# Optimization experiments

Hardware: AMD Instinct MI355X
Metric: run time of the kernel (lower is better)

## Reference

```python
import jax, jax.numpy as jnp
import numpy as np

INPUT_SIZE = 64
HIDDEN = 128
NUM_CLASSES = 4
BATCH = 512
SEQ = 1024


def setup_inputs() -> dict:
    key = jax.random.key(0)
    ks = jax.random.split(key, 11)
    s_in = 1.0 / np.sqrt(INPUT_SIZE)
    s_h = 1.0 / np.sqrt(HIDDEN)
    inp = {
        "x": jax.random.normal(ks[0], (BATCH, SEQ, INPUT_SIZE), dtype=jnp.float32),
        # layer1: x_proj (4H, in), h_proj (4H, H), each with bias
        "Wx1": jax.random.uniform(ks[1], (4 * HIDDEN, INPUT_SIZE), minval=-s_in, maxval=s_in),
        "bx1": jax.random.uniform(ks[2], (4 * HIDDEN,), minval=-s_in, maxval=s_in),
        "Wh1": jax.random.uniform(ks[3], (4 * HIDDEN, HIDDEN), minval=-s_h, maxval=s_h),
        "bh1": jax.random.uniform(ks[4], (4 * HIDDEN,), minval=-s_h, maxval=s_h),
        # layer2: x_proj (4H, H), h_proj (4H, H)
        "Wx2": jax.random.uniform(ks[5], (4 * HIDDEN, HIDDEN), minval=-s_h, maxval=s_h),
        "bx2": jax.random.uniform(ks[6], (4 * HIDDEN,), minval=-s_h, maxval=s_h),
        "Wh2": jax.random.uniform(ks[7], (4 * HIDDEN, HIDDEN), minval=-s_h, maxval=s_h),
        "bh2": jax.random.uniform(ks[8], (4 * HIDDEN,), minval=-s_h, maxval=s_h),
        # classifier head (num_classes, H)
        "Wc": jax.random.uniform(ks[9], (NUM_CLASSES, HIDDEN), minval=-s_h, maxval=s_h),
        "bc": jax.random.uniform(ks[10], (NUM_CLASSES,), minval=-s_h, maxval=s_h),
    }
    return inp


def _cell(gates, c_prev):
    # torch Linear gate order after chunk(4): i, f, g, o
    i, f, g, o = jnp.split(gates, 4, axis=-1)
    c = jax.nn.sigmoid(f) * c_prev + jax.nn.sigmoid(i) * jnp.tanh(g)
    h = jax.nn.sigmoid(o) * jnp.tanh(c)
    return h, c


def reference(x, Wx1, bx1, Wh1, bh1, Wx2, bx2, Wh2, bh2, Wc, bc):
    B = x.shape[0]
    H = Wh1.shape[1]
    # Precompute input projections for all timesteps in one big GEMM: (B,S,4H)
    xg1 = jnp.einsum("bsi,gi->bsg", x, Wx1) + bx1 + bh1  # fold both biases
    xg1_t = jnp.swapaxes(xg1, 0, 1)  # (S, B, 4H) for scan

    def step(carry, xg_t):
        h1, c1, h2, c2 = carry
        gates1 = xg_t + h1 @ Wh1.T
        h1, c1 = _cell(gates1, c1)
        gates2 = h1 @ Wx2.T + bx2 + h2 @ Wh2.T + bh2
        h2, c2 = _cell(gates2, c2)
        return (h1, c1, h2, c2), None

    z = jnp.zeros((B, H), dtype=x.dtype)
    (h1, c1, h2, c2), _ = jax.lax.scan(step, (z, z, z, z), xg1_t)
    logits = h2 @ Wc.T + bc  # (B, num_classes)
    return logits
```

## Files before the change

### kernel.cpp

```cpp
#include <hip/hip_runtime.h>
#include <hip/hip_fp16.h>

namespace {

constexpr int kS = 1024;
constexpr int kI = 64;
constexpr int kH = 128;

typedef _Float16 f16x8 __attribute__((ext_vector_type(8)));
typedef float    f32x4 __attribute__((ext_vector_type(4)));

#define MFMA16(a, b, c) __builtin_amdgcn_mfma_f32_16x16x32_f16((a), (b), (c), 0, 0, 0)

__device__ __forceinline__ float rcpf(float x) {
#if __has_builtin(__builtin_amdgcn_rcpf)
  return __builtin_amdgcn_rcpf(x);
#else
  return 1.0f / x;
#endif
}
__device__ __forceinline__ float sigf(float x)  { return rcpf(1.0f + __expf(-x)); }
__device__ __forceinline__ float tanhff(float x){ return 1.0f - 2.0f * rcpf(1.0f + __expf(2.0f * x)); }

template <int P>
__device__ __forceinline__ void prio() {
#if __has_builtin(__builtin_amdgcn_s_setprio)
  __builtin_amdgcn_s_setprio(P);
#endif
}

__device__ __forceinline__ unsigned packf2(float lo, float hi) {
  _Float16 a = (_Float16)lo, b = (_Float16)hi;
  unsigned short ua = __builtin_bit_cast(unsigned short, a);
  unsigned short ub = __builtin_bit_cast(unsigned short, b);
  return (unsigned)ua | ((unsigned)ub << 16);
}

__device__ __forceinline__ f16x8 afrag(const float* __restrict__ W, int row,
                                       int k0, int ld) {
  const float4* p = reinterpret_cast<const float4*>(W + (size_t)row * ld + k0);
  const float4 u = p[0], v = p[1];
  f16x8 a;
  a[0] = (_Float16)u.x; a[1] = (_Float16)u.y; a[2] = (_Float16)u.z; a[3] = (_Float16)u.w;
  a[4] = (_Float16)v.x; a[5] = (_Float16)v.y; a[6] = (_Float16)v.z; a[7] = (_Float16)v.w;
  return a;
}

__global__ __launch_bounds__(1024) void lstm_l1(
    const float* __restrict__ x, const float* __restrict__ Wx1,
    const float* __restrict__ bx1, const float* __restrict__ Wh1,
    const float* __restrict__ bh1, _Float16* __restrict__ h1out)
{
  const int tid  = threadIdx.x;
  const int b0   = blockIdx.x * 2;
  const int w    = tid >> 6;
  const int lane = tid & 63;
  const int q    = lane >> 4;
  const int n    = lane & 15;

  __shared__ __align__(16) _Float16 xF[8][16][8];
  __shared__ __align__(16) _Float16 h1B[2][2][16][8];
  __shared__ float xg[512][17];
  __shared__ float gbuf[2][512];

  f16x8 Ax[2][2], Ah[2][4];
  {
    const int rb = w * 32 + n;
#pragma unroll
    for (int s = 0; s < 2; ++s) {
      const int row = rb + s * 16;
#pragma unroll
      for (int kt = 0; kt < 2; ++kt) Ax[s][kt] = afrag(Wx1, row, kt * 32 + q * 8, kI);
#pragma unroll
      for (int kt = 0; kt < 4; ++kt) Ah[s][kt] = afrag(Wh1, row, kt * 32 + q * 8, kH);
    }
  }

  float bI = 0.f, bF = 0.f, bG = 0.f, bO = 0.f, cst = 0.f;
  if (tid < 256) {
    const int j = tid & 127;
    bI = bx1[j]       + bh1[j];
    bF = bx1[j + 128] + bh1[j + 128];
    bG = bx1[j + 256] + bh1[j + 256];
    bO = bx1[j + 384] + bh1[j + 384];
    reinterpret_cast<_Float16*>(&h1B[1][0][0][0])[tid] = (_Float16)0.f;
  }

  const int csel  = (n < 2) ? n : 0;
  const char* h1base = reinterpret_cast<const char*>(&h1B[0][0][0][0]);

  for (int t0 = 0; t0 < kS; t0 += 8) {
    if (tid < 512) {
      const int col = tid >> 5, sk2 = tid & 31;
      const int c = col & 1, dt = col >> 1;
      const float2 v = *reinterpret_cast<const float2*>(
          x + ((size_t)(b0 + c) * kS + (size_t)(t0 + dt)) * kI + sk2 * 2);
      const int k = sk2 * 2;
      *reinterpret_cast<unsigned*>(&xF[k >> 3][col][k & 7]) = packf2(v.x, v.y);
    }
    __syncthreads();

    {
      const char* xb = reinterpret_cast<const char*>(&xF[0][0][0]);
      f32x4 e0 = {0.f, 0.f, 0.f, 0.f}, e1 = {0.f, 0.f, 0.f, 0.f};
#pragma unroll
      for (int kt = 0; kt < 2; ++kt) {
        const f16x8 bf = *reinterpret_cast<const f16x8*>(
            xb + (((kt * 4 + q) * 16 + n) << 4));
        e0 = MFMA16(Ax[0][kt], bf, e0);
        e1 = MFMA16(Ax[1][kt], bf, e1);
      }
#pragma unroll
      for (int r = 0; r < 4; ++r) {
        xg[w * 32 + q * 4 + r][n]      = e0[r];
        xg[w * 32 + 16 + q * 4 + r][n] = e1[r];
      }
    }
    __syncthreads();

    for (int dt = 0; dt < 8; ++dt) {
      const int t = t0 + dt;
      const int rp = (t + 1) & 1;
      const char* hb = h1base + ((rp * 2 + csel) << 8);

      f32x4 d0 = {0.f, 0.f, 0.f, 0.f}, d1 = {0.f, 0.f, 0.f, 0.f};
      prio<1>();
#pragma unroll
      for (int kt = 0; kt < 4; ++kt) {
        const f16x8 bf = *reinterpret_cast<const f16x8*>(hb + ((kt * 4 + q) << 4));
        d0 = MFMA16(Ah[0][kt], bf, d0);
        d1 = MFMA16(Ah[1][kt], bf, d1);
      }
      prio<0>();

      if (n < 2) {
        *reinterpret_cast<f32x4*>(&gbuf[n][w * 32 + q * 4])      = d0;
        *reinterpret_cast<f32x4*>(&gbuf[n][w * 32 + 16 + q * 4]) = d1;
      }
      __syncthreads();

      if (tid < 256) {
        const int c = tid >> 7, j = tid & 127, col = dt * 2 + c;
        const float gi = xg[j][col]       + gbuf[c][j]       + bI;
        const float gf = xg[j + 128][col] + gbuf[c][j + 128] + bF;
        const float gg = xg[j + 256][col] + gbuf[c][j + 256] + bG;
        const float go = xg[j + 384][col] + gbuf[c][j + 384] + bO;
        cst = sigf(gf) * cst + sigf(gi) * tanhff(gg);
        const float h = sigf(go) * tanhff(cst);
        h1B[t & 1][c][j >> 3][j & 7] = (_Float16)h;
        h1out[((size_t)(b0 + c) * kS + (size_t)t) * kH + j] = (_Float16)h;
      }
      __syncthreads();
    }
  }
}

__global__ __launch_bounds__(1024) void lstm_l2(
    const _Float16* __restrict__ h1in,
    const float* __restrict__ Wx2, const float* __restrict__ bx2,
    const float* __restrict__ Wh2, const float* __restrict__ bh2,
    const float* __restrict__ Wc,  const float* __restrict__ bc,
    float* __restrict__ out)
{
  const int tid  = threadIdx.x;
  const int b0   = blockIdx.x * 2;
  const int w    = tid >> 6;
  const int lane = tid & 63;
  const int q    = lane >> 4;
  const int n    = lane & 15;

  __shared__ __align__(16) _Float16 h1F[16][16][8];
  __shared__ __align__(16) _Float16 h2B[2][2][16][8];
  __shared__ float xg[512][17];
  __shared__ float gbuf[2][512];
  __shared__ float hfin[2][128];

  f16x8 Ax[2][4], Ah[2][4];
  {
    const int rb = w * 32 + n;
#pragma unroll
    for (int s = 0; s < 2; ++s) {
      const int row = rb + s * 16;
#pragma unroll
      for (int kt = 0; kt < 4; ++kt) {
        Ax[s][kt] = afrag(Wx2, row, kt * 32 + q * 8, kH);
        Ah[s][kt] = afrag(Wh2, row, kt * 32 + q * 8, kH);
      }
    }
  }

  float bI = 0.f, bF = 0.f, bG = 0.f, bO = 0.f, cst = 0.f;
  if (tid < 256) {
    const int j = tid & 127;
    bI = bx2[j]       + bh2[j];
    bF = bx2[j + 128] + bh2[j + 128];
    bG = bx2[j + 256] + bh2[j + 256];
    bO = bx2[j + 384] + bh2[j + 384];
    reinterpret_cast<_Float16*>(&h2B[1][0][0][0])[tid] = (_Float16)0.f;
  }

  const int csel = (n < 2) ? n : 0;
  const char* h2base = reinterpret_cast<const char*>(&h2B[0][0][0][0]);

  for (int t0 = 0; t0 < kS; t0 += 8) {
    {
      const int col = tid >> 6, sk2 = tid & 63;
      const int c = col & 1, dt = col >> 1;
      const unsigned v = *reinterpret_cast<const unsigned*>(
          h1in + ((size_t)(b0 + c) * kS + (size_t)(t0 + dt)) * kH + sk2 * 2);
      const int k = sk2 * 2;
      *reinterpret_cast<unsigned*>(&h1F[k >> 3][col][k & 7]) = v;
    }
    __syncthreads();

    {
      const char* xb = reinterpret_cast<const char*>(&h1F[0][0][0]);
      f32x4 e0 = {0.f, 0.f, 0.f, 0.f}, e1 = {0.f, 0.f, 0.f, 0.f};
#pragma unroll
      for (int kt = 0; kt < 4; ++kt) {
        const f16x8 bf = *reinterpret_cast<const f16x8*>(
            xb + (((kt * 4 + q) * 16 + n) << 4));
        e0 = MFMA16(Ax[0][kt], bf, e0);
        e1 = MFMA16(Ax[1][kt], bf, e1);
      }
#pragma unroll
      for (int r = 0; r < 4; ++r) {
        xg[w * 32 + q * 4 + r][n]      = e0[r];
        xg[w * 32 + 16 + q * 4 + r][n] = e1[r];
      }
    }
    __syncthreads();

    for (int dt = 0; dt < 8; ++dt) {
      const int t = t0 + dt;
      const int rp = (t + 1) & 1;
      const char* hb = h2base + ((rp * 2 + csel) << 8);

      f32x4 d0 = {0.f, 0.f, 0.f, 0.f}, d1 = {0.f, 0.f, 0.f, 0.f};
      prio<1>();
#pragma unroll
      for (int kt = 0; kt < 4; ++kt) {
        const f16x8 bf = *reinterpret_cast<const f16x8*>(hb + ((kt * 4 + q) << 4));
        d0 = MFMA16(Ah[0][kt], bf, d0);
        d1 = MFMA16(Ah[1][kt], bf, d1);
      }
      prio<0>();

      if (n < 2) {
        *reinterpret_cast<f32x4*>(&gbuf[n][w * 32 + q * 4])      = d0;
        *reinterpret_cast<f32x4*>(&gbuf[n][w * 32 + 16 + q * 4]) = d1;
      }
      __syncthreads();

      if (tid < 256) {
        const int c = tid >> 7, j = tid & 127, col = dt * 2 + c;
        const float gi = xg[j][col]       + gbuf[c][j]       + bI;
        const float gf = xg[j + 128][col] + gbuf[c][j + 128] + bF;
        const float gg = xg[j + 256][col] + gbuf[c][j + 256] + bG;
        const float go = xg[j + 384][col] + gbuf[c][j + 384] + bO;
        cst = sigf(gf) * cst + sigf(gi) * tanhff(gg);
        const float h = sigf(go) * tanhff(cst);
        h2B[t & 1][c][j >> 3][j & 7] = (_Float16)h;
        if (t == kS - 1) hfin[c][j] = h;
      }
      __syncthreads();
    }
  }

  if (tid < 8) {
    const int m = tid & 3, c = tid >> 2;
    const float* wr = Wc + (size_t)m * kH;
    float s0 = 0.f, s1 = 0.f, s2 = 0.f, s3 = 0.f;
#pragma unroll
    for (int j = 0; j < kH; j += 4) {
      s0 = fmaf(wr[j],     hfin[c][j],     s0);
      s1 = fmaf(wr[j + 1], hfin[c][j + 1], s1);
      s2 = fmaf(wr[j + 2], hfin[c][j + 2], s2);
      s3 = fmaf(wr[j + 3], hfin[c][j + 3], s3);
    }
    out[(size_t)(b0 + c) * 4 + m] = bc[m] + ((s0 + s1) + (s2 + s3));
  }
}

}

extern "C" void kernel_launch(void* const* d_in, const int* in_sizes, int n_in,
                              void* d_out, int out_size, void* d_ws, size_t ws_size,
                              hipStream_t stream) {
  const float* x   = (const float*)d_in[0];
  const float* Wx1 = (const float*)d_in[1];
  const float* bx1 = (const float*)d_in[2];
  const float* Wh1 = (const float*)d_in[3];
  const float* bh1 = (const float*)d_in[4];
  const float* Wx2 = (const float*)d_in[5];
  const float* bx2 = (const float*)d_in[6];
  const float* Wh2 = (const float*)d_in[7];
  const float* bh2 = (const float*)d_in[8];
  const float* Wc  = (const float*)d_in[9];
  const float* bc  = (const float*)d_in[10];

  _Float16* h1 = (_Float16*)d_ws;

  hipLaunchKernelGGL(lstm_l1, dim3(256), dim3(1024), 0, stream,
                     x, Wx1, bx1, Wh1, bh1, h1);
  hipLaunchKernelGGL(lstm_l2, dim3(256), dim3(1024), 0, stream,
                     h1, Wx2, bx2, Wh2, bh2, Wc, bc, (float*)d_out);
}
```

Measured before the change: 1.537 ms.

## Remap gate rows per wave so each lane owns i,f,g,o and drop a barrier

Each block drops from 16 to 8 waves, and each wave now computes all four gates for the same 16 hidden units. The lanes holding the MFMA output can then apply the LSTM cell directly in registers, without staging gate sums through shared memory and a second barrier per timestep. The precomputed input projection is stored transposed so each lane reads its four values as one vector, and the s_setprio hints are removed. In exchange, each wave holds twice as many weight fragments in registers, and only the lanes with n<2 run the elementwise math, so each of them does four hidden units serially.

```diff
diff --git a/kernel.cpp b/kernel.cpp
--- a/kernel.cpp
+++ b/kernel.cpp
@@ -21,13 +21,6 @@
 }
 __device__ __forceinline__ float sigf(float x)  { return rcpf(1.0f + __expf(-x)); }
 __device__ __forceinline__ float tanhff(float x){ return 1.0f - 2.0f * rcpf(1.0f + __expf(2.0f * x)); }
-
-template <int P>
-__device__ __forceinline__ void prio() {
-#if __has_builtin(__builtin_amdgcn_s_setprio)
-  __builtin_amdgcn_s_setprio(P);
-#endif
-}
 
 __device__ __forceinline__ unsigned packf2(float lo, float hi) {
   _Float16 a = (_Float16)lo, b = (_Float16)hi;
@@ -46,7 +39,8 @@
   return a;
 }
 
-__global__ __launch_bounds__(1024) void lstm_l1(
+
+__global__ __launch_bounds__(512) void lstm_l1(
     const float* __restrict__ x, const float* __restrict__ Wx1,
     const float* __restrict__ bx1, const float* __restrict__ Wh1,
     const float* __restrict__ bh1, _Float16* __restrict__ h1out)
@@ -57,105 +51,104 @@
   const int lane = tid & 63;
   const int q    = lane >> 4;
   const int n    = lane & 15;
+  const int j0   = 16 * w + 4 * q;
 
   __shared__ __align__(16) _Float16 xF[8][16][8];
   __shared__ __align__(16) _Float16 h1B[2][2][16][8];
-  __shared__ float xg[512][17];
-  __shared__ float gbuf[2][512];
-
-  f16x8 Ax[2][2], Ah[2][4];
-  {
-    const int rb = w * 32 + n;
-#pragma unroll
-    for (int s = 0; s < 2; ++s) {
-      const int row = rb + s * 16;
-#pragma unroll
-      for (int kt = 0; kt < 2; ++kt) Ax[s][kt] = afrag(Wx1, row, kt * 32 + q * 8, kI);
-#pragma unroll
-      for (int kt = 0; kt < 4; ++kt) Ah[s][kt] = afrag(Wh1, row, kt * 32 + q * 8, kH);
-    }
-  }
-
-  float bI = 0.f, bF = 0.f, bG = 0.f, bO = 0.f, cst = 0.f;
-  if (tid < 256) {
-    const int j = tid & 127;
-    bI = bx1[j]       + bh1[j];
-    bF = bx1[j + 128] + bh1[j + 128];
-    bG = bx1[j + 256] + bh1[j + 256];
-    bO = bx1[j + 384] + bh1[j + 384];
-    reinterpret_cast<_Float16*>(&h1B[1][0][0][0])[tid] = (_Float16)0.f;
-  }
-
-  const int csel  = (n < 2) ? n : 0;
+  __shared__ float xg2[16][516];
+
+  f16x8 Ax[4][2], Ah[4][4];
+#pragma unroll
+  for (int g = 0; g < 4; ++g) {
+    const int row = g * 128 + 16 * w + n;
+#pragma unroll
+    for (int kt = 0; kt < 2; ++kt) Ax[g][kt] = afrag(Wx1, row, kt * 32 + q * 8, kI);
+#pragma unroll
+    for (int kt = 0; kt < 4; ++kt) Ah[g][kt] = afrag(Wh1, row, kt * 32 + q * 8, kH);
+  }
+
+  f32x4 bI4, bF4, bG4, bO4;
+#pragma unroll
+  for (int r = 0; r < 4; ++r) {
+    bI4[r] = bx1[j0 + r]       + bh1[j0 + r];
+    bF4[r] = bx1[j0 + 128 + r] + bh1[j0 + 128 + r];
+    bG4[r] = bx1[j0 + 256 + r] + bh1[j0 + 256 + r];
+    bO4[r] = bx1[j0 + 384 + r] + bh1[j0 + 384 + r];
+  }
+  if (tid < 256) reinterpret_cast<_Float16*>(&h1B[1][0][0][0])[tid] = (_Float16)0.f;
+
+  f32x4 cst = {0.f, 0.f, 0.f, 0.f};
+  const int csel = (n < 2) ? n : 0;
   const char* h1base = reinterpret_cast<const char*>(&h1B[0][0][0][0]);
 
   for (int t0 = 0; t0 < kS; t0 += 8) {
-    if (tid < 512) {
-      const int col = tid >> 5, sk2 = tid & 31;
-      const int c = col & 1, dt = col >> 1;
+    {
+      const int col = tid >> 5, k2 = tid & 31;
+      const int c = col & 1, dt = col >> 1, k = k2 * 2;
       const float2 v = *reinterpret_cast<const float2*>(
-          x + ((size_t)(b0 + c) * kS + (size_t)(t0 + dt)) * kI + sk2 * 2);
-      const int k = sk2 * 2;
+          x + ((size_t)(b0 + c) * kS + (size_t)(t0 + dt)) * kI + k);
       *reinterpret_cast<unsigned*>(&xF[k >> 3][col][k & 7]) = packf2(v.x, v.y);
     }
     __syncthreads();
 
     {
       const char* xb = reinterpret_cast<const char*>(&xF[0][0][0]);
-      f32x4 e0 = {0.f, 0.f, 0.f, 0.f}, e1 = {0.f, 0.f, 0.f, 0.f};
+      f32x4 e0 = {0,0,0,0}, e1 = {0,0,0,0}, e2 = {0,0,0,0}, e3 = {0,0,0,0};
 #pragma unroll
       for (int kt = 0; kt < 2; ++kt) {
         const f16x8 bf = *reinterpret_cast<const f16x8*>(
             xb + (((kt * 4 + q) * 16 + n) << 4));
-        e0 = MFMA16(Ax[0][kt], bf, e0);
-        e1 = MFMA16(Ax[1][kt], bf, e1);
-      }
-#pragma unroll
-      for (int r = 0; r < 4; ++r) {
-        xg[w * 32 + q * 4 + r][n]      = e0[r];
-        xg[w * 32 + 16 + q * 4 + r][n] = e1[r];
-      }
+        e0 = MFMA16(Ax[0][kt], bf, e0);  e1 = MFMA16(Ax[1][kt], bf, e1);
+        e2 = MFMA16(Ax[2][kt], bf, e2);  e3 = MFMA16(Ax[3][kt], bf, e3);
+      }
+      *reinterpret_cast<f32x4*>(&xg2[n][j0])       = e0;
+      *reinterpret_cast<f32x4*>(&xg2[n][j0 + 128]) = e1;
+      *reinterpret_cast<f32x4*>(&xg2[n][j0 + 256]) = e2;
+      *reinterpret_cast<f32x4*>(&xg2[n][j0 + 384]) = e3;
     }
     __syncthreads();
 
     for (int dt = 0; dt < 8; ++dt) {
       const int t = t0 + dt;
-      const int rp = (t + 1) & 1;
-      const char* hb = h1base + ((rp * 2 + csel) << 8);
-
-      f32x4 d0 = {0.f, 0.f, 0.f, 0.f}, d1 = {0.f, 0.f, 0.f, 0.f};
-      prio<1>();
+      const char* hb = h1base + ((((t + 1) & 1) * 2 + csel) << 8);
+
+      f32x4 d0 = {0,0,0,0}, d1 = {0,0,0,0}, d2 = {0,0,0,0}, d3 = {0,0,0,0};
 #pragma unroll
       for (int kt = 0; kt < 4; ++kt) {
         const f16x8 bf = *reinterpret_cast<const f16x8*>(hb + ((kt * 4 + q) << 4));
-        d0 = MFMA16(Ah[0][kt], bf, d0);
-        d1 = MFMA16(Ah[1][kt], bf, d1);
-      }
-      prio<0>();
+        d0 = MFMA16(Ah[0][kt], bf, d0);  d1 = MFMA16(Ah[1][kt], bf, d1);
+        d2 = MFMA16(Ah[2][kt], bf, d2);  d3 = MFMA16(Ah[3][kt], bf, d3);
+      }
 
       if (n < 2) {
-        *reinterpret_cast<f32x4*>(&gbuf[n][w * 32 + q * 4])      = d0;
-        *reinterpret_cast<f32x4*>(&gbuf[n][w * 32 + 16 + q * 4]) = d1;
+        const int col = dt * 2 + n;
+        const f32x4 xa  = *reinterpret_cast<const f32x4*>(&xg2[col][j0]);
+        const f32x4 xf  = *reinterpret_cast<const f32x4*>(&xg2[col][j0 + 128]);
+        const f32x4 xgg = *reinterpret_cast<const f32x4*>(&xg2[col][j0 + 256]);
+        const f32x4 xo  = *reinterpret_cast<const f32x4*>(&xg2[col][j0 + 384]);
+        float h[4];
+#pragma unroll
+        for (int r = 0; r < 4; ++r) {
+          const float gi = d0[r] + xa[r]  + bI4[r];
+          const float gf = d1[r] + xf[r]  + bF4[r];
+          const float gg = d2[r] + xgg[r] + bG4[r];
+          const float go = d3[r] + xo[r]  + bO4[r];
+          cst[r] = sigf(gf) * cst[r] + sigf(gi) * tanhff(gg);
+          h[r] = sigf(go) * tanhff(cst[r]);
+        }
+        uint2 hp;
+        hp.x = packf2(h[0], h[1]);
+        hp.y = packf2(h[2], h[3]);
+        *reinterpret_cast<uint2*>(&h1B[t & 1][n][j0 >> 3][j0 & 7]) = hp;
+        *reinterpret_cast<uint2*>(
+            h1out + ((size_t)(b0 + n) * kS + (size_t)t) * kH + j0) = hp;
       }
       __syncthreads();
-
-      if (tid < 256) {
-        const int c = tid >> 7, j = tid & 127, col = dt * 2 + c;
-        const float gi = xg[j][col]       + gbuf[c][j]       + bI;
-        const float gf = xg[j + 128][col] + gbuf[c][j + 128] + bF;
-        const float gg = xg[j + 256][col] + gbuf[c][j + 256] + bG;
-        const float go = xg[j + 384][col] + gbuf[c][j + 384] + bO;
-        cst = sigf(gf) * cst + sigf(gi) * tanhff(gg);
-        const float h = sigf(go) * tanhff(cst);
-        h1B[t & 1][c][j >> 3][j & 7] = (_Float16)h;
-        h1out[((size_t)(b0 + c) * kS + (size_t)t) * kH + j] = (_Float16)h;
-      }
-      __syncthreads();
-    }
-  }
-}
-
-__global__ __launch_bounds__(1024) void lstm_l2(
+    }
+  }
+}
+
+__global__ __launch_bounds__(512) void lstm_l2(
     const _Float16* __restrict__ h1in,
     const float* __restrict__ Wx2, const float* __restrict__ bx2,
     const float* __restrict__ Wh2, const float* __restrict__ bh2,
@@ -168,100 +161,101 @@
   const int lane = tid & 63;
   const int q    = lane >> 4;
   const int n    = lane & 15;
+  const int j0   = 16 * w + 4 * q;
 
   __shared__ __align__(16) _Float16 h1F[16][16][8];
   __shared__ __align__(16) _Float16 h2B[2][2][16][8];
-  __shared__ float xg[512][17];
-  __shared__ float gbuf[2][512];
+  __shared__ float xg2[16][516];
   __shared__ float hfin[2][128];
 
-  f16x8 Ax[2][4], Ah[2][4];
-  {
-    const int rb = w * 32 + n;
-#pragma unroll
-    for (int s = 0; s < 2; ++s) {
-      const int row = rb + s * 16;
-#pragma unroll
-      for (int kt = 0; kt < 4; ++kt) {
-        Ax[s][kt] = afrag(Wx2, row, kt * 32 + q * 8, kH);
-        Ah[s][kt] = afrag(Wh2, row, kt * 32 + q * 8, kH);
-      }
-    }
-  }
-
-  float bI = 0.f, bF = 0.f, bG = 0.f, bO = 0.f, cst = 0.f;
-  if (tid < 256) {
-    const int j = tid & 127;
-    bI = bx2[j]       + bh2[j];
-    bF = bx2[j + 128] + bh2[j + 128];
-    bG = bx2[j + 256] + bh2[j + 256];
-    bO = bx2[j + 384] + bh2[j + 384];
-    reinterpret_cast<_Float16*>(&h2B[1][0][0][0])[tid] = (_Float16)0.f;
-  }
-
+  f16x8 Ax[4][4], Ah[4][4];
+#pragma unroll
+  for (int g = 0; g < 4; ++g) {
+    const int row = g * 128 + 16 * w + n;
+#pragma unroll
+    for (int kt = 0; kt < 4; ++kt) {
+      Ax[g][kt] = afrag(Wx2, row, kt * 32 + q * 8, kH);
+      Ah[g][kt] = afrag(Wh2, row, kt * 32 + q * 8, kH);
+    }
+  }
+
+  f32x4 bI4, bF4, bG4, bO4;
+#pragma unroll
+  for (int r = 0; r < 4; ++r) {
+    bI4[r] = bx2[j0 + r]       + bh2[j0 + r];
+    bF4[r] = bx2[j0 + 128 + r] + bh2[j0 + 128 + r];
+    bG4[r] = bx2[j0 + 256 + r] + bh2[j0 + 256 + r];
+    bO4[r] = bx2[j0 + 384 + r] + bh2[j0 + 384 + r];
+  }
+  if (tid < 256) reinterpret_cast<_Float16*>(&h2B[1][0][0][0])[tid] = (_Float16)0.f;
+
+  f32x4 cst = {0.f, 0.f, 0.f, 0.f};
   const int csel = (n < 2) ? n : 0;
   const char* h2base = reinterpret_cast<const char*>(&h2B[0][0][0][0]);
 
   for (int t0 = 0; t0 < kS; t0 += 8) {
     {
-      const int col = tid >> 6, sk2 = tid & 63;
-      const int c = col & 1, dt = col >> 1;
-      const unsigned v = *reinterpret_cast<const unsigned*>(
-          h1in + ((size_t)(b0 + c) * kS + (size_t)(t0 + dt)) * kH + sk2 * 2);
-      const int k = sk2 * 2;
-      *reinterpret_cast<unsigned*>(&h1F[k >> 3][col][k & 7]) = v;
+      const int col = tid >> 5, quad = tid & 31;
+      const int c = col & 1, dt = col >> 1, k = quad * 4;
+      const uint2 v = *reinterpret_cast<const uint2*>(
+          h1in + ((size_t)(b0 + c) * kS + (size_t)(t0 + dt)) * kH + k);
+      *reinterpret_cast<uint2*>(&h1F[k >> 3][col][k & 7]) = v;
     }
     __syncthreads();
 
     {
       const char* xb = reinterpret_cast<const char*>(&h1F[0][0][0]);
-      f32x4 e0 = {0.f, 0.f, 0.f, 0.f}, e1 = {0.f, 0.f, 0.f, 0.f};
+      f32x4 e0 = {0,0,0,0}, e1 = {0,0,0,0}, e2 = {0,0,0,0}, e3 = {0,0,0,0};
 #pragma unroll
       for (int kt = 0; kt < 4; ++kt) {
         const f16x8 bf = *reinterpret_cast<const f16x8*>(
             xb + (((kt * 4 + q) * 16 + n) << 4));
-        e0 = MFMA16(Ax[0][kt], bf, e0);
-        e1 = MFMA16(Ax[1][kt], bf, e1);
-      }
-#pragma unroll
-      for (int r = 0; r < 4; ++r) {
-        xg[w * 32 + q * 4 + r][n]      = e0[r];
-        xg[w * 32 + 16 + q * 4 + r][n] = e1[r];
-      }
+        e0 = MFMA16(Ax[0][kt], bf, e0);  e1 = MFMA16(Ax[1][kt], bf, e1);
+        e2 = MFMA16(Ax[2][kt], bf, e2);  e3 = MFMA16(Ax[3][kt], bf, e3);
+      }
+      *reinterpret_cast<f32x4*>(&xg2[n][j0])       = e0;
+      *reinterpret_cast<f32x4*>(&xg2[n][j0 + 128]) = e1;
+      *reinterpret_cast<f32x4*>(&xg2[n][j0 + 256]) = e2;
+      *reinterpret_cast<f32x4*>(&xg2[n][j0 + 384]) = e3;
     }
     __syncthreads();
 
     for (int dt = 0; dt < 8; ++dt) {
       const int t = t0 + dt;
-      const int rp = (t + 1) & 1;
-      const char* hb = h2base + ((rp * 2 + csel) << 8);
-
-      f32x4 d0 = {0.f, 0.f, 0.f, 0.f}, d1 = {0.f, 0.f, 0.f, 0.f};
-      prio<1>();
+      const char* hb = h2base + ((((t + 1) & 1) * 2 + csel) << 8);
+
+      f32x4 d0 = {0,0,0,0}, d1 = {0,0,0,0}, d2 = {0,0,0,0}, d3 = {0,0,0,0};
 #pragma unroll
       for (int kt = 0; kt < 4; ++kt) {
         const f16x8 bf = *reinterpret_cast<const f16x8*>(hb + ((kt * 4 + q) << 4));
-        d0 = MFMA16(Ah[0][kt], bf, d0);
-        d1 = MFMA16(Ah[1][kt], bf, d1);
-      }
-      prio<0>();
+        d0 = MFMA16(Ah[0][kt], bf, d0);  d1 = MFMA16(Ah[1][kt], bf, d1);
+        d2 = MFMA16(Ah[2][kt], bf, d2);  d3 = MFMA16(Ah[3][kt], bf, d3);
+      }
 
       if (n < 2) {
-        *reinterpret_cast<f32x4*>(&gbuf[n][w * 32 + q * 4])      = d0;
-        *reinterpret_cast<f32x4*>(&gbuf[n][w * 32 + 16 + q * 4]) = d1;
-      }
-      __syncthreads();
-
-      if (tid < 256) {
-        const int c = tid >> 7, j = tid & 127, col = dt * 2 + c;
-        const float gi = xg[j][col]       + gbuf[c][j]       + bI;
-        const float gf = xg[j + 128][col] + gbuf[c][j + 128] + bF;
-        const float gg = xg[j + 256][col] + gbuf[c][j + 256] + bG;
-        const float go = xg[j + 384][col] + gbuf[c][j + 384] + bO;
-        cst = sigf(gf) * cst + sigf(gi) * tanhff(gg);
-        const float h = sigf(go) * tanhff(cst);
-        h2B[t & 1][c][j >> 3][j & 7] = (_Float16)h;
-        if (t == kS - 1) hfin[c][j] = h;
+        const int col = dt * 2 + n;
+        const f32x4 xa  = *reinterpret_cast<const f32x4*>(&xg2[col][j0]);
+        const f32x4 xf  = *reinterpret_cast<const f32x4*>(&xg2[col][j0 + 128]);
+        const f32x4 xgg = *reinterpret_cast<const f32x4*>(&xg2[col][j0 + 256]);
+        const f32x4 xo  = *reinterpret_cast<const f32x4*>(&xg2[col][j0 + 384]);
+        float h[4];
+#pragma unroll
+        for (int r = 0; r < 4; ++r) {
+          const float gi = d0[r] + xa[r]  + bI4[r];
+          const float gf = d1[r] + xf[r]  + bF4[r];
+          const float gg = d2[r] + xgg[r] + bG4[r];
+          const float go = d3[r] + xo[r]  + bO4[r];
+          cst[r] = sigf(gf) * cst[r] + sigf(gi) * tanhff(gg);
+          h[r] = sigf(go) * tanhff(cst[r]);
+        }
+        uint2 hp;
+        hp.x = packf2(h[0], h[1]);
+        hp.y = packf2(h[2], h[3]);
+        *reinterpret_cast<uint2*>(&h2B[t & 1][n][j0 >> 3][j0 & 7]) = hp;
+        if (t == kS - 1) {
+          f32x4 hv = {h[0], h[1], h[2], h[3]};
+          *reinterpret_cast<f32x4*>(&hfin[n][j0]) = hv;
+        }
       }
       __syncthreads();
     }
@@ -301,8 +295,8 @@
 
   _Float16* h1 = (_Float16*)d_ws;
 
-  hipLaunchKernelGGL(lstm_l1, dim3(256), dim3(1024), 0, stream,
+  hipLaunchKernelGGL(lstm_l1, dim3(256), dim3(512), 0, stream,
                      x, Wx1, bx1, Wh1, bh1, h1);
-  hipLaunchKernelGGL(lstm_l2, dim3(256), dim3(1024), 0, stream,
+  hipLaunchKernelGGL(lstm_l2, dim3(256), dim3(512), 0, stream,
                      h1, Wx2, bx2, Wh2, bh2, Wc, bc, (float*)d_out);
 }
```

Result: slower. 2.151 ms (+40.0%).

## Fuse both LSTM layers into one wavefront-specialized kernel with layer-2 lagging one chunk

Applied to the files above, without the earlier changes.

Merges the two per-layer kernels into a single kernel. Waves 0-7 run layer 1 and waves 8-15 run layer 2, with layer 2 one 8-step chunk behind. Layer-1 hidden states pass through shared memory instead of a global fp16 buffer, and each step's two recurrences share the same barriers. This removes the global round-trip of h1 and roughly halves the number of serial barrier-bound steps. In exchange, each wave now holds more recurrent weight fragments in registers, the input-projection weights are reloaded from global memory every chunk, and the setprio hints are dropped.

```diff
diff --git a/kernel.cpp b/kernel.cpp
--- a/kernel.cpp
+++ b/kernel.cpp
@@ -21,20 +21,6 @@
 }
 __device__ __forceinline__ float sigf(float x)  { return rcpf(1.0f + __expf(-x)); }
 __device__ __forceinline__ float tanhff(float x){ return 1.0f - 2.0f * rcpf(1.0f + __expf(2.0f * x)); }
-
-template <int P>
-__device__ __forceinline__ void prio() {
-#if __has_builtin(__builtin_amdgcn_s_setprio)
-  __builtin_amdgcn_s_setprio(P);
-#endif
-}
-
-__device__ __forceinline__ unsigned packf2(float lo, float hi) {
-  _Float16 a = (_Float16)lo, b = (_Float16)hi;
-  unsigned short ua = __builtin_bit_cast(unsigned short, a);
-  unsigned short ub = __builtin_bit_cast(unsigned short, b);
-  return (unsigned)ua | ((unsigned)ub << 16);
-}
 
 __device__ __forceinline__ f16x8 afrag(const float* __restrict__ W, int row,
                                        int k0, int ld) {
@@ -46,117 +32,11 @@
   return a;
 }
 
-__global__ __launch_bounds__(1024) void lstm_l1(
-    const float* __restrict__ x, const float* __restrict__ Wx1,
-    const float* __restrict__ bx1, const float* __restrict__ Wh1,
-    const float* __restrict__ bh1, _Float16* __restrict__ h1out)
-{
-  const int tid  = threadIdx.x;
-  const int b0   = blockIdx.x * 2;
-  const int w    = tid >> 6;
-  const int lane = tid & 63;
-  const int q    = lane >> 4;
-  const int n    = lane & 15;
-
-  __shared__ __align__(16) _Float16 xF[8][16][8];
-  __shared__ __align__(16) _Float16 h1B[2][2][16][8];
-  __shared__ float xg[512][17];
-  __shared__ float gbuf[2][512];
-
-  f16x8 Ax[2][2], Ah[2][4];
-  {
-    const int rb = w * 32 + n;
-#pragma unroll
-    for (int s = 0; s < 2; ++s) {
-      const int row = rb + s * 16;
-#pragma unroll
-      for (int kt = 0; kt < 2; ++kt) Ax[s][kt] = afrag(Wx1, row, kt * 32 + q * 8, kI);
-#pragma unroll
-      for (int kt = 0; kt < 4; ++kt) Ah[s][kt] = afrag(Wh1, row, kt * 32 + q * 8, kH);
-    }
-  }
-
-  float bI = 0.f, bF = 0.f, bG = 0.f, bO = 0.f, cst = 0.f;
-  if (tid < 256) {
-    const int j = tid & 127;
-    bI = bx1[j]       + bh1[j];
-    bF = bx1[j + 128] + bh1[j + 128];
-    bG = bx1[j + 256] + bh1[j + 256];
-    bO = bx1[j + 384] + bh1[j + 384];
-    reinterpret_cast<_Float16*>(&h1B[1][0][0][0])[tid] = (_Float16)0.f;
-  }
-
-  const int csel  = (n < 2) ? n : 0;
-  const char* h1base = reinterpret_cast<const char*>(&h1B[0][0][0][0]);
-
-  for (int t0 = 0; t0 < kS; t0 += 8) {
-    if (tid < 512) {
-      const int col = tid >> 5, sk2 = tid & 31;
-      const int c = col & 1, dt = col >> 1;
-      const float2 v = *reinterpret_cast<const float2*>(
-          x + ((size_t)(b0 + c) * kS + (size_t)(t0 + dt)) * kI + sk2 * 2);
-      const int k = sk2 * 2;
-      *reinterpret_cast<unsigned*>(&xF[k >> 3][col][k & 7]) = packf2(v.x, v.y);
-    }
-    __syncthreads();
-
-    {
-      const char* xb = reinterpret_cast<const char*>(&xF[0][0][0]);
-      f32x4 e0 = {0.f, 0.f, 0.f, 0.f}, e1 = {0.f, 0.f, 0.f, 0.f};
-#pragma unroll
-      for (int kt = 0; kt < 2; ++kt) {
-        const f16x8 bf = *reinterpret_cast<const f16x8*>(
-            xb + (((kt * 4 + q) * 16 + n) << 4));
-        e0 = MFMA16(Ax[0][kt], bf, e0);
-        e1 = MFMA16(Ax[1][kt], bf, e1);
-      }
-#pragma unroll
-      for (int r = 0; r < 4; ++r) {
-        xg[w * 32 + q * 4 + r][n]      = e0[r];
-        xg[w * 32 + 16 + q * 4 + r][n] = e1[r];
-      }
-    }
-    __syncthreads();
-
-    for (int dt = 0; dt < 8; ++dt) {
-      const int t = t0 + dt;
-      const int rp = (t + 1) & 1;
-      const char* hb = h1base + ((rp * 2 + csel) << 8);
-
-      f32x4 d0 = {0.f, 0.f, 0.f, 0.f}, d1 = {0.f, 0.f, 0.f, 0.f};
-      prio<1>();
-#pragma unroll
-      for (int kt = 0; kt < 4; ++kt) {
-        const f16x8 bf = *reinterpret_cast<const f16x8*>(hb + ((kt * 4 + q) << 4));
-        d0 = MFMA16(Ah[0][kt], bf, d0);
-        d1 = MFMA16(Ah[1][kt], bf, d1);
-      }
-      prio<0>();
-
-      if (n < 2) {
-        *reinterpret_cast<f32x4*>(&gbuf[n][w * 32 + q * 4])      = d0;
-        *reinterpret_cast<f32x4*>(&gbuf[n][w * 32 + 16 + q * 4]) = d1;
-      }
-      __syncthreads();
-
-      if (tid < 256) {
-        const int c = tid >> 7, j = tid & 127, col = dt * 2 + c;
-        const float gi = xg[j][col]       + gbuf[c][j]       + bI;
-        const float gf = xg[j + 128][col] + gbuf[c][j + 128] + bF;
-        const float gg = xg[j + 256][col] + gbuf[c][j + 256] + bG;
-        const float go = xg[j + 384][col] + gbuf[c][j + 384] + bO;
-        cst = sigf(gf) * cst + sigf(gi) * tanhff(gg);
-        const float h = sigf(go) * tanhff(cst);
-        h1B[t & 1][c][j >> 3][j & 7] = (_Float16)h;
-        h1out[((size_t)(b0 + c) * kS + (size_t)t) * kH + j] = (_Float16)h;
-      }
-      __syncthreads();
-    }
-  }
-}
-
-__global__ __launch_bounds__(1024) void lstm_l2(
-    const _Float16* __restrict__ h1in,
+__global__ __launch_bounds__(1024, 1) __attribute__((amdgpu_waves_per_eu(4, 4)))
+void lstm_fused(
+    const float* __restrict__ x,
+    const float* __restrict__ Wx1, const float* __restrict__ bx1,
+    const float* __restrict__ Wh1, const float* __restrict__ bh1,
     const float* __restrict__ Wx2, const float* __restrict__ bx2,
     const float* __restrict__ Wh2, const float* __restrict__ bh2,
     const float* __restrict__ Wc,  const float* __restrict__ bc,
@@ -168,100 +48,154 @@
   const int lane = tid & 63;
   const int q    = lane >> 4;
   const int n    = lane & 15;
-
-  __shared__ __align__(16) _Float16 h1F[16][16][8];
+  const int lw   = w & 7;
+  const bool isL2w = (w >= 8);
+  const int csel = (n < 2) ? n : 0;
+
+  __shared__ __align__(16) _Float16 xF[8][17][8];
+  __shared__ __align__(16) _Float16 h1R[2][16][17][8];
   __shared__ __align__(16) _Float16 h2B[2][2][16][8];
-  __shared__ float xg[512][17];
-  __shared__ float gbuf[2][512];
+  __shared__ float xg1[16][516];
+  __shared__ float xg2[16][516];
+  __shared__ float g1[2][512];
+  __shared__ float g2[2][512];
   __shared__ float hfin[2][128];
 
-  f16x8 Ax[2][4], Ah[2][4];
+  f16x8 Ah[4][4];
   {
-    const int rb = w * 32 + n;
-#pragma unroll
-    for (int s = 0; s < 2; ++s) {
-      const int row = rb + s * 16;
-#pragma unroll
-      for (int kt = 0; kt < 4; ++kt) {
-        Ax[s][kt] = afrag(Wx2, row, kt * 32 + q * 8, kH);
-        Ah[s][kt] = afrag(Wh2, row, kt * 32 + q * 8, kH);
-      }
-    }
+    const float* Wr = isL2w ? Wh2 : Wh1;
+#pragma unroll
+    for (int i = 0; i < 4; ++i)
+#pragma unroll
+      for (int kt = 0; kt < 4; ++kt)
+        Ah[i][kt] = afrag(Wr, (lw * 4 + i) * 16 + n, kt * 32 + q * 8, kH);
   }
 
   float bI = 0.f, bF = 0.f, bG = 0.f, bO = 0.f, cst = 0.f;
   if (tid < 256) {
+    const int j = tid & 127;
+    bI = bx1[j]       + bh1[j];
+    bF = bx1[j + 128] + bh1[j + 128];
+    bG = bx1[j + 256] + bh1[j + 256];
+    bO = bx1[j + 384] + bh1[j + 384];
+  } else if (tid >= 512 && tid < 768) {
     const int j = tid & 127;
     bI = bx2[j]       + bh2[j];
     bF = bx2[j + 128] + bh2[j + 128];
     bG = bx2[j + 256] + bh2[j + 256];
     bO = bx2[j + 384] + bh2[j + 384];
-    reinterpret_cast<_Float16*>(&h2B[1][0][0][0])[tid] = (_Float16)0.f;
-  }
-
-  const int csel = (n < 2) ? n : 0;
-  const char* h2base = reinterpret_cast<const char*>(&h2B[0][0][0][0]);
-
-  for (int t0 = 0; t0 < kS; t0 += 8) {
-    {
-      const int col = tid >> 6, sk2 = tid & 63;
+  }
+
+  for (int i = tid; i < 16 * 17 * 8; i += 1024)
+    (&h1R[1][0][0][0])[i] = (_Float16)0.f;
+  if (tid < 512) (&h2B[0][0][0][0])[tid] = (_Float16)0.f;
+
+  for (int T = 0; T < 129; ++T) {
+    const bool hasL1 = (T < 128);
+    const bool hasL2 = (T > 0);
+
+    if (hasL1) {
+      const int col = tid >> 6, k = tid & 63;
       const int c = col & 1, dt = col >> 1;
-      const unsigned v = *reinterpret_cast<const unsigned*>(
-          h1in + ((size_t)(b0 + c) * kS + (size_t)(t0 + dt)) * kH + sk2 * 2);
-      const int k = sk2 * 2;
-      *reinterpret_cast<unsigned*>(&h1F[k >> 3][col][k & 7]) = v;
+      xF[k >> 3][col][k & 7] =
+          (_Float16)x[((size_t)(b0 + c) * kS + (size_t)(T * 8 + dt)) * kI + k];
     }
     __syncthreads();
 
-    {
-      const char* xb = reinterpret_cast<const char*>(&h1F[0][0][0]);
-      f32x4 e0 = {0.f, 0.f, 0.f, 0.f}, e1 = {0.f, 0.f, 0.f, 0.f};
+    if (!isL2w && hasL1) {
+      f32x4 e0 = {0,0,0,0}, e1 = {0,0,0,0}, e2 = {0,0,0,0}, e3 = {0,0,0,0};
+      const char* xb = reinterpret_cast<const char*>(&xF[0][0][0]);
+#pragma unroll
+      for (int kt = 0; kt < 2; ++kt) {
+        const f16x8 bf = *reinterpret_cast<const f16x8*>(
+            xb + (((kt * 4 + q) * 17 + n) << 4));
+        e0 = MFMA16(afrag(Wx1, (lw*4+0)*16 + n, kt*32 + q*8, kI), bf, e0);
+        e1 = MFMA16(afrag(Wx1, (lw*4+1)*16 + n, kt*32 + q*8, kI), bf, e1);
+        e2 = MFMA16(afrag(Wx1, (lw*4+2)*16 + n, kt*32 + q*8, kI), bf, e2);
+        e3 = MFMA16(afrag(Wx1, (lw*4+3)*16 + n, kt*32 + q*8, kI), bf, e3);
+      }
+      *reinterpret_cast<f32x4*>(&xg1[n][(lw*4+0)*16 + q*4]) = e0;
+      *reinterpret_cast<f32x4*>(&xg1[n][(lw*4+1)*16 + q*4]) = e1;
+      *reinterpret_cast<f32x4*>(&xg1[n][(lw*4+2)*16 + q*4]) = e2;
+      *reinterpret_cast<f32x4*>(&xg1[n][(lw*4+3)*16 + q*4]) = e3;
+    }
+    if (isL2w && hasL2) {
+      f32x4 e0 = {0,0,0,0}, e1 = {0,0,0,0}, e2 = {0,0,0,0}, e3 = {0,0,0,0};
+      const char* hb = reinterpret_cast<const char*>(&h1R[(T + 1) & 1][0][0][0]);
 #pragma unroll
       for (int kt = 0; kt < 4; ++kt) {
         const f16x8 bf = *reinterpret_cast<const f16x8*>(
-            xb + (((kt * 4 + q) * 16 + n) << 4));
-        e0 = MFMA16(Ax[0][kt], bf, e0);
-        e1 = MFMA16(Ax[1][kt], bf, e1);
-      }
-#pragma unroll
-      for (int r = 0; r < 4; ++r) {
-        xg[w * 32 + q * 4 + r][n]      = e0[r];
-        xg[w * 32 + 16 + q * 4 + r][n] = e1[r];
-      }
+            hb + (((kt * 4 + q) * 17 + n) << 4));
+        e0 = MFMA16(afrag(Wx2, (lw*4+0)*16 + n, kt*32 + q*8, kH), bf, e0);
+        e1 = MFMA16(afrag(Wx2, (lw*4+1)*16 + n, kt*32 + q*8, kH), bf, e1);
+        e2 = MFMA16(afrag(Wx2, (lw*4+2)*16 + n, kt*32 + q*8, kH), bf, e2);
+        e3 = MFMA16(afrag(Wx2, (lw*4+3)*16 + n, kt*32 + q*8, kH), bf, e3);
+      }
+      *reinterpret_cast<f32x4*>(&xg2[n][(lw*4+0)*16 + q*4]) = e0;
+      *reinterpret_cast<f32x4*>(&xg2[n][(lw*4+1)*16 + q*4]) = e1;
+      *reinterpret_cast<f32x4*>(&xg2[n][(lw*4+2)*16 + q*4]) = e2;
+      *reinterpret_cast<f32x4*>(&xg2[n][(lw*4+3)*16 + q*4]) = e3;
     }
     __syncthreads();
 
     for (int dt = 0; dt < 8; ++dt) {
-      const int t = t0 + dt;
-      const int rp = (t + 1) & 1;
-      const char* hb = h2base + ((rp * 2 + csel) << 8);
-
-      f32x4 d0 = {0.f, 0.f, 0.f, 0.f}, d1 = {0.f, 0.f, 0.f, 0.f};
-      prio<1>();
-#pragma unroll
-      for (int kt = 0; kt < 4; ++kt) {
-        const f16x8 bf = *reinterpret_cast<const f16x8*>(hb + ((kt * 4 + q) << 4));
-        d0 = MFMA16(Ah[0][kt], bf, d0);
-        d1 = MFMA16(Ah[1][kt], bf, d1);
-      }
-      prio<0>();
-
-      if (n < 2) {
-        *reinterpret_cast<f32x4*>(&gbuf[n][w * 32 + q * 4])      = d0;
-        *reinterpret_cast<f32x4*>(&gbuf[n][w * 32 + 16 + q * 4]) = d1;
+      const int t  = T * 8 + dt;
+      const int t2 = t - 8;
+
+      if (!isL2w && hasL1) {
+        const int rb  = (dt == 0) ? ((T + 1) & 1) : (T & 1);
+        const int col = (dt == 0) ? (14 + csel) : ((dt - 1) * 2 + csel);
+        const char* hb = reinterpret_cast<const char*>(&h1R[rb][0][0][0]) + col * 16;
+        f32x4 d0 = {0,0,0,0}, d1 = {0,0,0,0}, d2 = {0,0,0,0}, d3 = {0,0,0,0};
+#pragma unroll
+        for (int kt = 0; kt < 4; ++kt) {
+          const f16x8 bf = *reinterpret_cast<const f16x8*>(hb + (kt * 4 + q) * 272);
+          d0 = MFMA16(Ah[0][kt], bf, d0);  d1 = MFMA16(Ah[1][kt], bf, d1);
+          d2 = MFMA16(Ah[2][kt], bf, d2);  d3 = MFMA16(Ah[3][kt], bf, d3);
+        }
+        if (n < 2) {
+          *reinterpret_cast<f32x4*>(&g1[n][(lw*4+0)*16 + q*4]) = d0;
+          *reinterpret_cast<f32x4*>(&g1[n][(lw*4+1)*16 + q*4]) = d1;
+          *reinterpret_cast<f32x4*>(&g1[n][(lw*4+2)*16 + q*4]) = d2;
+          *reinterpret_cast<f32x4*>(&g1[n][(lw*4+3)*16 + q*4]) = d3;
+        }
+      }
+      if (isL2w && hasL2) {
+        const char* hb = reinterpret_cast<const char*>(&h2B[(t2 + 1) & 1][csel][0][0]);
+        f32x4 d0 = {0,0,0,0}, d1 = {0,0,0,0}, d2 = {0,0,0,0}, d3 = {0,0,0,0};
+#pragma unroll
+        for (int kt = 0; kt < 4; ++kt) {
+          const f16x8 bf = *reinterpret_cast<const f16x8*>(hb + ((kt * 4 + q) << 4));
+          d0 = MFMA16(Ah[0][kt], bf, d0);  d1 = MFMA16(Ah[1][kt], bf, d1);
+          d2 = MFMA16(Ah[2][kt], bf, d2);  d3 = MFMA16(Ah[3][kt], bf, d3);
+        }
+        if (n < 2) {
+          *reinterpret_cast<f32x4*>(&g2[n][(lw*4+0)*16 + q*4]) = d0;
+          *reinterpret_cast<f32x4*>(&g2[n][(lw*4+1)*16 + q*4]) = d1;
+          *reinterpret_cast<f32x4*>(&g2[n][(lw*4+2)*16 + q*4]) = d2;
+          *reinterpret_cast<f32x4*>(&g2[n][(lw*4+3)*16 + q*4]) = d3;
+        }
       }
       __syncthreads();
 
-      if (tid < 256) {
+      if (tid < 256 && hasL1) {
         const int c = tid >> 7, j = tid & 127, col = dt * 2 + c;
-        const float gi = xg[j][col]       + gbuf[c][j]       + bI;
-        const float gf = xg[j + 128][col] + gbuf[c][j + 128] + bF;
-        const float gg = xg[j + 256][col] + gbuf[c][j + 256] + bG;
-        const float go = xg[j + 384][col] + gbuf[c][j + 384] + bO;
+        const float gi = xg1[col][j]       + g1[c][j]       + bI;
+        const float gf = xg1[col][j + 128] + g1[c][j + 128] + bF;
+        const float gg = xg1[col][j + 256] + g1[c][j + 256] + bG;
+        const float go = xg1[col][j + 384] + g1[c][j + 384] + bO;
+        cst = sigf(gf) * cst + sigf(gi) * tanhff(gg);
+        h1R[T & 1][j >> 3][col][j & 7] = (_Float16)(sigf(go) * tanhff(cst));
+      } else if (tid >= 512 && tid < 768 && hasL2) {
+        const int c = (tid >> 7) & 1, j = tid & 127, col = dt * 2 + c;
+        const float gi = xg2[col][j]       + g2[c][j]       + bI;
+        const float gf = xg2[col][j + 128] + g2[c][j + 128] + bF;
+        const float gg = xg2[col][j + 256] + g2[c][j + 256] + bG;
+        const float go = xg2[col][j + 384] + g2[c][j + 384] + bO;
         cst = sigf(gf) * cst + sigf(gi) * tanhff(gg);
         const float h = sigf(go) * tanhff(cst);
-        h2B[t & 1][c][j >> 3][j & 7] = (_Float16)h;
-        if (t == kS - 1) hfin[c][j] = h;
+        h2B[t2 & 1][c][j >> 3][j & 7] = (_Float16)h;
+        if (t2 == kS - 1) hfin[c][j] = h;
       }
       __syncthreads();
     }
@@ -299,10 +233,7 @@
   const float* Wc  = (const float*)d_in[9];
   const float* bc  = (const float*)d_in[10];
 
-  _Float16* h1 = (_Float16*)d_ws;
-
-  hipLaunchKernelGGL(lstm_l1, dim3(256), dim3(1024), 0, stream,
-                     x, Wx1, bx1, Wh1, bh1, h1);
-  hipLaunchKernelGGL(lstm_l2, dim3(256), dim3(1024), 0, stream,
-                     h1, Wx2, bx2, Wh2, bh2, Wc, bc, (float*)d_out);
-}
+  hipLaunchKernelGGL(lstm_fused, dim3(256), dim3(1024), 0, stream,
+                     x, Wx1, bx1, Wh1, bh1, Wx2, bx2, Wh2, bh2, Wc, bc,
+                     (float*)d_out);
+}
```

Measured after the change: 3.042 ms. 98.0% more time.
